# Optimization experiments

Hardware: AMD Instinct MI355X
Metric: run time of the kernel (lower is better)

## Reference

```python
import jax, jax.numpy as jnp
import numpy as np

N, E, F, H = 50000, 500000, 128, 128   # nodes, edges, in-features, hidden
L, R, B = 3, 8, 30                     # layers, relations, bases
G, C = 16, 8                           # graphs in batch, classes
EPS = 1e-5


def setup_inputs() -> dict:
    key = jax.random.key(0)
    ks = jax.random.split(key, 16)
    x = jax.random.normal(ks[0], (N, F), jnp.float32)
    edge_index = jax.random.randint(ks[1], (2, E), 0, N)
    edge_attr = jax.random.randint(ks[2], (E,), 0, R)
    batch = jnp.sort(jax.random.randint(ks[3], (N,), 0, G))
    # RGCN params (all layers share shapes since F == H)
    basis = jax.random.normal(ks[4], (L, B, H, H), jnp.float32) * 0.05
    comp = jax.random.normal(ks[5], (L, R, B), jnp.float32) * 0.2
    root = jax.random.normal(ks[6], (L, H, H), jnp.float32) * 0.05
    bias = jnp.zeros((L, H), jnp.float32)
    # BatchNorm (eval mode: running stats)
    bn1_gamma = jnp.ones((F,), jnp.float32)
    bn1_beta = jnp.zeros((F,), jnp.float32)
    bn1_mean = jax.random.normal(ks[7], (F,), jnp.float32) * 0.1
    bn1_var = jax.random.uniform(ks[8], (F,), jnp.float32, 0.5, 1.5)
    bn2_gamma = jnp.ones((H,), jnp.float32)
    bn2_beta = jnp.zeros((H,), jnp.float32)
    bn2_mean = jax.random.normal(ks[9], (H,), jnp.float32) * 0.1
    bn2_var = jax.random.uniform(ks[10], (H,), jnp.float32, 0.5, 1.5)
    fc1_w = jax.random.normal(ks[11], (H, H), jnp.float32) * 0.05
    fc1_b = jnp.zeros((H,), jnp.float32)
    fc2_w = jax.random.normal(ks[12], (H, C), jnp.float32) * 0.05
    fc2_b = jnp.zeros((C,), jnp.float32)
    return dict(x=x, edge_index=edge_index, edge_attr=edge_attr, batch=batch,
                bn1_gamma=bn1_gamma, bn1_beta=bn1_beta, bn1_mean=bn1_mean, bn1_var=bn1_var,
                basis=basis, comp=comp, root=root, bias=bias,
                bn2_gamma=bn2_gamma, bn2_beta=bn2_beta, bn2_mean=bn2_mean, bn2_var=bn2_var,
                fc1_w=fc1_w, fc1_b=fc1_b, fc2_w=fc2_w, fc2_b=fc2_b)


def _bn(x, gamma, beta, mean, var):
    return (x - mean) * jax.lax.rsqrt(var + EPS) * gamma + beta


def _rgcn_layer(x, basis_l, comp_l, root_l, bias_l, src, dst, edge_attr):
    # root transform + bias
    out = x @ root_l + bias_l
    # relation-wise basis-decomposed message passing, mean-aggregated per relation
    for r in range(R):
        W_r = jnp.einsum('b,bio->io', comp_l[r], basis_l)  # [H, H]
        xw = x @ W_r                                       # [N, H]
        mask = (edge_attr == r).astype(x.dtype)            # [E]
        msg = xw[src] * mask[:, None]                      # gather + mask
        agg = jax.ops.segment_sum(msg, dst, num_segments=N)
        deg = jax.ops.segment_sum(mask, dst, num_segments=N)
        out = out + agg / jnp.maximum(deg, 1.0)[:, None]
    return out


def reference(x, edge_index, edge_attr, batch,
              bn1_gamma, bn1_beta, bn1_mean, bn1_var,
              basis, comp, root, bias,
              bn2_gamma, bn2_beta, bn2_mean, bn2_var,
              fc1_w, fc1_b, fc2_w, fc2_b):
    src, dst = edge_index[0], edge_index[1]
    h = _bn(x, bn1_gamma, bn1_beta, bn1_mean, bn1_var)
    for l in range(L):
        h = jax.nn.relu(_rgcn_layer(h, basis[l], comp[l], root[l], bias[l], src, dst, edge_attr))
        # dropout is identity in eval mode
    # global mean pool per graph
    sums = jax.ops.segment_sum(h, batch, num_segments=G)            # [G, H]
    counts = jax.ops.segment_sum(jnp.ones((N,), h.dtype), batch, num_segments=G)
    g = sums / jnp.maximum(counts, 1.0)[:, None]
    g = _bn(g, bn2_gamma, bn2_beta, bn2_mean, bn2_var)
    # temporal_type == 'mean'
    v = jax.nn.relu(g.mean(axis=0))                                 # [H]
    v = jax.nn.relu(v @ fc1_w + fc1_b)
    logits = v @ fc2_w + fc2_b                                      # [C]
    return jax.nn.log_softmax(logits, axis=-1)
```

## Files before the change

kernel.cpp:

```cpp
#include <hip/hip_runtime.h>
#include <hip/hip_bf16.h>

#define NN 50000
#define NE 500000
#define HID 128
#define LAYERS 3
#define RELS 8
#define BASES 30
#define GRAPHS 16
#define CLASSES 8
#define EPSV 1e-5f
#define NOUT (HID * (RELS + 1))
#define SCAN_CHUNK 1024
#define SCAN_NBLK ((NN + SCAN_CHUNK - 1) / SCAN_CHUNK)
#define PCHUNK 128
#define NSTRIPE ((NN + 127) / 128)
#define NSG ((NSTRIPE + 7) / 8)

typedef __attribute__((ext_vector_type(8))) short short8;
typedef __attribute__((ext_vector_type(4))) float f32x4;
typedef __attribute__((ext_vector_type(2))) float f32x2;

__device__ __forceinline__ float bf2f(unsigned short u) {
    union { unsigned int i; float f; } x; x.i = ((unsigned int)u) << 16; return x.f;
}
__device__ __forceinline__ unsigned short f2bf(float f) {
    __hip_bfloat16 b = __float2bfloat16(f);
    return *(unsigned short*)&b;
}
template <bool HI>
__device__ __forceinline__ f32x2 fp8x2_2f(int u) {
    return __builtin_amdgcn_cvt_pk_f32_fp8(u, HI);
}
__device__ __forceinline__ int permf(int f) {
    return (f & 64) | ((f & 15) << 2) | ((f >> 4) & 3);
}
__device__ __forceinline__ int ipermf(int q) {
    return (q & 64) | ((q & 3) << 4) | ((q >> 2) & 15);
}
__device__ __forceinline__ void gload16(const void* g, void* l) {
    __builtin_amdgcn_global_load_lds(
        (const __attribute__((address_space(1))) unsigned int*)g,
        (__attribute__((address_space(3))) unsigned int*)l, 16, 0, 0);
}

__global__ __launch_bounds__(256) void build_wcat(const float* __restrict__ basis,
                                                  const float* __restrict__ comp,
                                                  const float* __restrict__ root,
                                                  unsigned short* __restrict__ wT) {
    int bid = blockIdx.x;
    int l = bid >> 6;
    int k0 = (bid & 63) << 1;
    __shared__ float cl[RELS * BASES];
    int tid = threadIdx.x;
    if (tid < RELS * BASES) cl[tid] = comp[l * RELS * BASES + tid];
    __syncthreads();
    int j = tid & 127;
    int k = k0 + (tid >> 7);
    int pk = permf(k);
    const float* bp = basis + ((size_t)l * BASES * HID + k) * HID + j;
    float acc[RELS];
#pragma unroll
    for (int r = 0; r < RELS; ++r) acc[r] = 0.f;
    for (int b = 0; b < BASES; ++b) {
        float v = bp[(size_t)b * HID * HID];
#pragma unroll
        for (int r = 0; r < RELS; ++r) acc[r] += cl[r * BASES + b] * v;
    }
    unsigned short* wl = wT + (size_t)l * NOUT * HID;
#pragma unroll
    for (int r = 0; r < RELS; ++r)
        wl[(size_t)((1 + r) * HID + j) * HID + pk] = f2bf(acc[r]);
    wl[(size_t)j * HID + pk] = f2bf(root[((size_t)l * HID + k) * HID + j]);
}

__global__ void bn1_kernel(const float* __restrict__ x, const float* __restrict__ gamma,
                           const float* __restrict__ beta, const float* __restrict__ mean,
                           const float* __restrict__ var, unsigned short* __restrict__ habf) {
    int idx = blockIdx.x * blockDim.x + threadIdx.x;
    if (idx >= NN * HID) return;
    int q = idx & (HID - 1);
    int n = idx >> 7;
    int f = ipermf(q);
    habf[idx] = f2bf((x[(n << 7) + f] - mean[f]) * rsqrtf(var[f] + EPSV) * gamma[f] + beta[f]);
}

__global__ void deg_kernel(const int* __restrict__ ei, const int* __restrict__ ea,
                           float* __restrict__ deg) {
    int e = blockIdx.x * blockDim.x + threadIdx.x;
    if (e >= NE) return;
    int dst = ei[NE + e];
    atomicAdd(&deg[(size_t)dst * RELS + ea[e]], 1.0f);
}

__global__ __launch_bounds__(256) void scan_partial(float* __restrict__ deg,
                                                    int* __restrict__ rowptr,
                                                    int* __restrict__ bsum) {
    __shared__ int ssc[256];
    int t = threadIdx.x;
    int base = blockIdx.x * SCAN_CHUNK + t * 4;
    int v[4];
#pragma unroll
    for (int j = 0; j < 4; ++j) {
        int node = base + j;
        if (node < NN) {
            float s = 0.f;
#pragma unroll
            for (int r = 0; r < RELS; ++r) {
                float d = deg[(size_t)node * RELS + r];
                s += d;
                deg[(size_t)node * RELS + r] = 1.0f / fmaxf(d, 1.0f);
            }
            v[j] = (int)(s + 0.5f);
        } else v[j] = 0;
    }
    int tsum = v[0] + v[1] + v[2] + v[3];
    ssc[t] = tsum;
    __syncthreads();
    for (int ofs = 1; ofs < 256; ofs <<= 1) {
        int add = (t >= ofs) ? ssc[t - ofs] : 0;
        __syncthreads();
        ssc[t] += add;
        __syncthreads();
    }
    int excl = ssc[t] - tsum;
    int e = 0;
#pragma unroll
    for (int j = 0; j < 4; ++j) {
        if (base + j < NN) rowptr[base + j] = excl + e;
        e += v[j];
    }
    if (t == 255) bsum[blockIdx.x] = ssc[255];
}

__global__ void scan_bsum(int* __restrict__ bsum) {
    if (threadIdx.x == 0) {
        int acc = 0;
        for (int b = 0; b < SCAN_NBLK; ++b) { int v = bsum[b]; bsum[b] = acc; acc += v; }
    }
}

__global__ __launch_bounds__(256) void scan_add(int* __restrict__ rowptr,
                                                const int* __restrict__ bsum) {
    int i = blockIdx.x * blockDim.x + threadIdx.x;
    if (i < NN) rowptr[i] += bsum[i >> 10];
    if (i == 0) rowptr[NN] = NE;
}

__global__ void fill_kernel(const int* __restrict__ ei, const int* __restrict__ ea,
                            const int* __restrict__ rowptr,
                            int* __restrict__ fillcnt, int* __restrict__ epk) {
    int e = blockIdx.x * blockDim.x + threadIdx.x;
    if (e >= NE) return;
    int src = ei[e];
    int dst = ei[NE + e];
    int r = ea[e];
    int pos = atomicAdd(&fillcnt[dst], 1);
    epk[rowptr[dst] + pos] = src | (r << 20);
}

__global__ __launch_bounds__(256) void gemm_mfma(const unsigned short* __restrict__ habf,
                                                 const unsigned short* __restrict__ wT,
                                                 const float* __restrict__ bias,
                                                 unsigned short* __restrict__ hnb,
                                                 unsigned char* __restrict__ xwb) {
    __shared__ __align__(16) unsigned short As[128 * 64];
    __shared__ __align__(16) unsigned short Bs[128 * 64];
    int bid = blockIdx.x;
    int sm8 = bid & 7;
    int rest = bid >> 3;
    int n0 = rest % (RELS + 1);
    int g = rest / (RELS + 1);
    int stripe = g * 8 + sm8;
    if (stripe >= NSTRIPE) return;
    int row0 = stripe * 128;

    int tid = threadIdx.x;
    int wave = tid >> 6, lane = tid & 63;
    int wm = (wave & 1) * 64, wn = (wave >> 1) * 64;
    int quad = lane >> 4, l16 = lane & 15;

    f32x4 acc[4][4];
#pragma unroll
    for (int i = 0; i < 4; ++i)
#pragma unroll
        for (int j = 0; j < 4; ++j) acc[i][j] = (f32x4){0.f, 0.f, 0.f, 0.f};

    int lr = lane >> 3;
    int lc = lane & 7;
    int sx = l16 & 7;

#pragma unroll
    for (int kh = 0; kh < 2; ++kh) {
#pragma unroll
        for (int q = 0; q < 4; ++q) {
            int rb = wave * 32 + q * 8;
            int r = rb + lr;
            int sc = (lc ^ (r & 7)) << 3;
            int ga = row0 + r; if (ga > NN - 1) ga = NN - 1;
            gload16(habf + (size_t)ga * HID + kh * 64 + sc, &As[rb * 64]);
            gload16(wT + (size_t)(n0 * 128 + r) * HID + kh * 64 + sc, &Bs[rb * 64]);
        }
        __syncthreads();
#pragma unroll
        for (int kc = 0; kc < 2; ++kc) {
            int ca = ((kc * 4 + quad) ^ sx) << 3;
            short8 a[4], b[4];
#pragma unroll
            for (int i = 0; i < 4; ++i) {
                a[i] = *(const short8*)&As[(wm + i * 16 + l16) * 64 + ca];
                b[i] = *(const short8*)&Bs[(wn + i * 16 + l16) * 64 + ca];
            }
#pragma unroll
            for (int i = 0; i < 4; ++i)
#pragma unroll
                for (int j = 0; j < 4; ++j)
                    acc[i][j] = __builtin_amdgcn_mfma_f32_16x16x32_bf16(a[i], b[j], acc[i][j], 0, 0, 0);
        }
        __syncthreads();
    }

    int pbase = wn + l16 * 4;
    if (n0 == 0) {
#pragma unroll
        for (int i = 0; i < 4; ++i)
#pragma unroll
            for (int reg = 0; reg < 4; ++reg) {
                int grow = row0 + wm + i * 16 + quad * 4 + reg;
                if (grow >= NN) continue;
                unsigned lo = (unsigned)f2bf(acc[i][0][reg] + bias[wn + l16]) |
                              ((unsigned)f2bf(acc[i][1][reg] + bias[wn + 16 + l16]) << 16);
                unsigned hi = (unsigned)f2bf(acc[i][2][reg] + bias[wn + 32 + l16]) |
                              ((unsigned)f2bf(acc[i][3][reg] + bias[wn + 48 + l16]) << 16);
                uint2 pk = {lo, hi};
                *(uint2*)(hnb + (size_t)grow * HID + pbase) = pk;
            }
    } else {
        int cbase = (n0 - 1) * 128;
#pragma unroll
        for (int i = 0; i < 4; ++i)
#pragma unroll
            for (int reg = 0; reg < 4; ++reg) {
                int grow = row0 + wm + i * 16 + quad * 4 + reg;
                if (grow >= NN) continue;
                unsigned w = (unsigned)__builtin_amdgcn_cvt_pk_fp8_f32(acc[i][0][reg], acc[i][1][reg], 0, false);
                w = (unsigned)__builtin_amdgcn_cvt_pk_fp8_f32(acc[i][2][reg], acc[i][3][reg], (int)w, true);
                *(unsigned*)(xwb + (size_t)grow * (RELS * HID) + cbase + pbase) = w;
            }
    }
}

__global__ __launch_bounds__(256) void aggregate_kernel(const int* __restrict__ rowptr,
                                                        const int* __restrict__ epk,
                                                        const float* __restrict__ invdeg,
                                                        const unsigned char* __restrict__ xwb,
                                                        const unsigned short* __restrict__ hnb,
                                                        unsigned short* __restrict__ habf) {
    int lane = threadIdx.x & 63;
    int half = lane >> 5;
    int hl = lane & 31;
    int node = (blockIdx.x << 3) + ((threadIdx.x >> 6) << 1) + half;
    if (node >= NN) return;
    int beg = rowptr[node], end = rowptr[node + 1];
    float dv = invdeg[(size_t)node * RELS + (hl & 7)];
    float a0 = 0.f, a1 = 0.f, a2 = 0.f, a3 = 0.f;
    int sbase = half << 5;
    for (int b0 = beg; b0 < end; b0 += 32) {
        int cnt = min(32, end - b0);
        int myp = 0;
        if (hl < cnt) myp = epk[b0 + hl];
        int j = 0;
        for (; j + 8 <= cnt; j += 8) {
            int p[8]; float s[8]; unsigned u[8];
#pragma unroll
            for (int t = 0; t < 8; ++t) p[t] = __shfl(myp, sbase + j + t);
#pragma unroll
            for (int t = 0; t < 8; ++t) s[t] = __shfl(dv, sbase + (p[t] >> 20));
#pragma unroll
            for (int t = 0; t < 8; ++t)
                u[t] = *(const unsigned*)(xwb + (size_t)(p[t] & 0xFFFFF) * (RELS * HID) + (p[t] >> 20) * HID + hl * 4);
#pragma unroll
            for (int t = 0; t < 8; ++t) {
                f32x2 lo = fp8x2_2f<false>((int)u[t]), hi = fp8x2_2f<true>((int)u[t]);
                a0 += lo.x * s[t]; a1 += lo.y * s[t]; a2 += hi.x * s[t]; a3 += hi.y * s[t];
            }
        }
        if (j + 4 <= cnt) {
            int p[4]; float s[4]; unsigned u[4];
#pragma unroll
            for (int t = 0; t < 4; ++t) p[t] = __shfl(myp, sbase + j + t);
#pragma unroll
            for (int t = 0; t < 4; ++t) s[t] = __shfl(dv, sbase + (p[t] >> 20));
#pragma unroll
            for (int t = 0; t < 4; ++t)
                u[t] = *(const unsigned*)(xwb + (size_t)(p[t] & 0xFFFFF) * (RELS * HID) + (p[t] >> 20) * HID + hl * 4);
#pragma unroll
            for (int t = 0; t < 4; ++t) {
                f32x2 lo = fp8x2_2f<false>((int)u[t]), hi = fp8x2_2f<true>((int)u[t]);
                a0 += lo.x * s[t]; a1 += lo.y * s[t]; a2 += hi.x * s[t]; a3 += hi.y * s[t];
            }
            j += 4;
        }
        for (; j < cnt; ++j) {
            int p = __shfl(myp, sbase + j);
            float s = __shfl(dv, sbase + (p >> 20));
            unsigned u = *(const unsigned*)(xwb + (size_t)(p & 0xFFFFF) * (RELS * HID) + (p >> 20) * HID + hl * 4);
            f32x2 lo = fp8x2_2f<false>((int)u), hi = fp8x2_2f<true>((int)u);
            a0 += lo.x * s; a1 += lo.y * s; a2 += hi.x * s; a3 += hi.y * s;
        }
    }
    const ushort2* hp = (const ushort2*)(hnb + (size_t)node * HID + hl * 4);
    ushort2 c0 = hp[0], c1 = hp[1];
    ushort2 o0, o1;
    o0.x = f2bf(fmaxf(bf2f(c0.x) + a0, 0.f));
    o0.y = f2bf(fmaxf(bf2f(c0.y) + a1, 0.f));
    o1.x = f2bf(fmaxf(bf2f(c1.x) + a2, 0.f));
    o1.y = f2bf(fmaxf(bf2f(c1.y) + a3, 0.f));
    ushort2* op = (ushort2*)(habf + (size_t)node * HID + hl * 4);
    op[0] = o0;
    op[1] = o1;
}

__global__ __launch_bounds__(256) void pool_kernel(const unsigned short* __restrict__ habf,
                                                   const int* __restrict__ batch,
                                                   float* __restrict__ psum,
                                                   float* __restrict__ pcnt) {
    int tid = threadIdx.x;
    int f = tid & 127;
    int sub = tid >> 7;
    int base = blockIdx.x * PCHUNK;
    float acc = 0.f, cnt = 0.f;
    int gcur = -1;
    for (int it = 0; it < PCHUNK / 2; ++it) {
        int node = base + it * 2 + sub;
        if (node >= NN) break;
        int g = batch[node];
        if (g != gcur) {
            if (gcur >= 0) {
                atomicAdd(&psum[gcur * HID + f], acc);
                if (f == 0) atomicAdd(&pcnt[gcur], cnt);
            }
            gcur = g; acc = 0.f; cnt = 0.f;
        }
        acc += bf2f(habf[(size_t)node * HID + f]);
        cnt += 1.f;
    }
    if (gcur >= 0) {
        atomicAdd(&psum[gcur * HID + f], acc);
        if (f == 0) atomicAdd(&pcnt[gcur], cnt);
    }
}

__global__ void head_kernel(const float* __restrict__ psum, const float* __restrict__ pcnt,
                            const float* __restrict__ g2, const float* __restrict__ b2,
                            const float* __restrict__ m2, const float* __restrict__ v2,
                            const float* __restrict__ fc1w, const float* __restrict__ fc1b,
                            const float* __restrict__ fc2w, const float* __restrict__ fc2b,
                            float* __restrict__ out) {
    __shared__ float v[HID];
    __shared__ float u[HID];
    __shared__ float lg[CLASSES];
    int j = threadIdx.x;
    int pj = permf(j);
    float acc = 0.f;
    for (int g = 0; g < GRAPHS; ++g) {
        float val = psum[g * HID + pj] / fmaxf(pcnt[g], 1.0f);
        val = (val - m2[j]) * rsqrtf(v2[j] + EPSV) * g2[j] + b2[j];
        acc += val;
    }
    v[j] = fmaxf(acc / (float)GRAPHS, 0.f);
    __syncthreads();
    float s = fc1b[j];
    for (int k = 0; k < HID; ++k) s += v[k] * fc1w[k * HID + j];
    u[j] = fmaxf(s, 0.f);
    __syncthreads();
    if (j < CLASSES) {
        float t = fc2b[j];
        for (int k = 0; k < HID; ++k) t += u[k] * fc2w[k * CLASSES + j];
        lg[j] = t;
    }
    __syncthreads();
    if (j < CLASSES) {
        float mx = lg[0];
        for (int c = 1; c < CLASSES; ++c) mx = fmaxf(mx, lg[c]);
        float se = 0.f;
        for (int c = 0; c < CLASSES; ++c) se += expf(lg[c] - mx);
        out[j] = lg[j] - mx - logf(se);
    }
}

extern "C" void kernel_launch(void* const* d_in, const int* in_sizes, int n_in,
                              void* d_out, int out_size, void* d_ws, size_t ws_size,
                              hipStream_t stream) {
    const float* x     = (const float*)d_in[0];
    const int*   ei    = (const int*)d_in[1];
    const int*   ea    = (const int*)d_in[2];
    const int*   batch = (const int*)d_in[3];
    const float* bn1g  = (const float*)d_in[4];
    const float* bn1b  = (const float*)d_in[5];
    const float* bn1m  = (const float*)d_in[6];
    const float* bn1v  = (const float*)d_in[7];
    const float* basis = (const float*)d_in[8];
    const float* comp  = (const float*)d_in[9];
    const float* root  = (const float*)d_in[10];
    const float* bias  = (const float*)d_in[11];
    const float* bn2g  = (const float*)d_in[12];
    const float* bn2b  = (const float*)d_in[13];
    const float* bn2m  = (const float*)d_in[14];
    const float* bn2v  = (const float*)d_in[15];
    const float* fc1w  = (const float*)d_in[16];
    const float* fc1b  = (const float*)d_in[17];
    const float* fc2w  = (const float*)d_in[18];
    const float* fc2b  = (const float*)d_in[19];

    float* ws = (float*)d_ws;
    size_t off = 0;
    unsigned short* wT = (unsigned short*)(ws + off); off += (size_t)LAYERS * NOUT * HID / 2;
    unsigned short* hnb  = (unsigned short*)(ws + off); off += (size_t)NN * HID / 2;
    unsigned short* habf = (unsigned short*)(ws + off); off += (size_t)NN * HID / 2;
    float* deg    = ws + off; off += (size_t)NN * RELS;
    float* psum   = ws + off; off += (size_t)GRAPHS * HID + GRAPHS;
    float* pcnt   = psum + GRAPHS * HID;
    int* rowptr   = (int*)(ws + off); off += (size_t)NN + 1;
    int* fillcnt  = (int*)(ws + off); off += (size_t)NN;
    int* bsum     = (int*)(ws + off); off += (size_t)SCAN_NBLK;
    int* epk      = (int*)(ws + off); off += (size_t)NE;
    off = (off + 3) & ~(size_t)3;
    unsigned char* xwb = (unsigned char*)(ws + off);
    off += (size_t)NN * RELS * HID / 4;
    if (ws_size < off * sizeof(float)) return;

    hipMemsetAsync(psum, 0, (GRAPHS * HID + GRAPHS) * sizeof(float), stream);
    hipMemsetAsync(deg, 0, (size_t)NN * RELS * sizeof(float), stream);
    hipMemsetAsync(fillcnt, 0, (size_t)NN * sizeof(int), stream);

    build_wcat<<<LAYERS * 64, 256, 0, stream>>>(basis, comp, root, wT);
    bn1_kernel<<<(NN * HID + 255) / 256, 256, 0, stream>>>(x, bn1g, bn1b, bn1m, bn1v, habf);

    deg_kernel<<<(NE + 255) / 256, 256, 0, stream>>>(ei, ea, deg);
    scan_partial<<<SCAN_NBLK, 256, 0, stream>>>(deg, rowptr, bsum);
    scan_bsum<<<1, 64, 0, stream>>>(bsum);
    scan_add<<<(NN + 255) / 256, 256, 0, stream>>>(rowptr, bsum);
    fill_kernel<<<(NE + 255) / 256, 256, 0, stream>>>(ei, ea, rowptr, fillcnt, epk);

    int gblocks = NSG * (RELS + 1) * 8;
    for (int l = 0; l < LAYERS; ++l) {
        gemm_mfma<<<gblocks, 256, 0, stream>>>(habf, wT + (size_t)l * NOUT * HID,
                                               bias + (size_t)l * HID, hnb, xwb);
        aggregate_kernel<<<(NN + 7) / 8, 256, 0, stream>>>(rowptr, epk, deg, xwb, hnb, habf);
    }

    pool_kernel<<<(NN + PCHUNK - 1) / PCHUNK, 256, 0, stream>>>(habf, batch, psum, pcnt);
    head_kernel<<<1, 128, 0, stream>>>(psum, pcnt, bn2g, bn2b, bn2m, bn2v,
                                       fc1w, fc1b, fc2w, fc2b, (float*)d_out);
}
```

Measured before the change: 397.1 us.

## Aggregate neighbor features per relation before transform in fused RGCN layer kernel

Replaces the transform-then-aggregate scheme (a GEMM writing 8 per-relation fp8 transformed features per node, then a gather kernel) with one fused kernel per layer. Each block of 64 destination nodes gathers and mean-aggregates raw bf16 neighbor features per relation using a (node,relation)-segmented CSR, then multiplies each aggregate by that relation's weight panel with MFMA, accumulating the root term, bias and ReLU in registers. This removes the large per-relation transformed-feature intermediate and its write and read traffic, and drops fp8 for bf16 inputs. In exchange each block runs nine serialized gather-then-MFMA phases with block barriers, has low occupancy given 48KB of LDS, and the CSR scan now covers eight times as many segments, so the bsum scan is widened to 512 threads.

New measurement: 488.8 us. 1.23x slower.

```diff
diff --git a/kernel.cpp b/kernel.cpp
--- a/kernel.cpp
+++ b/kernel.cpp
@@ -11,15 +11,15 @@
 #define CLASSES 8
 #define EPSV 1e-5f
 #define NOUT (HID * (RELS + 1))
+#define NSEG (NN * RELS)
 #define SCAN_CHUNK 1024
-#define SCAN_NBLK ((NN + SCAN_CHUNK - 1) / SCAN_CHUNK)
+#define SCAN_NBLK2 ((NSEG + SCAN_CHUNK - 1) / SCAN_CHUNK)
 #define PCHUNK 128
-#define NSTRIPE ((NN + 127) / 128)
-#define NSG ((NSTRIPE + 7) / 8)
+#define DTILE 64
+#define NDBLK ((NN + DTILE - 1) / DTILE)
 
 typedef __attribute__((ext_vector_type(8))) short short8;
 typedef __attribute__((ext_vector_type(4))) float f32x4;
-typedef __attribute__((ext_vector_type(2))) float f32x2;
 
 __device__ __forceinline__ float bf2f(unsigned short u) {
     union { unsigned int i; float f; } x; x.i = ((unsigned int)u) << 16; return x.f;
@@ -28,9 +28,11 @@
     __hip_bfloat16 b = __float2bfloat16(f);
     return *(unsigned short*)&b;
 }
-template <bool HI>
-__device__ __forceinline__ f32x2 fp8x2_2f(int u) {
-    return __builtin_amdgcn_cvt_pk_f32_fp8(u, HI);
+__device__ __forceinline__ float ubf_lo(unsigned w) {
+    union { unsigned i; float f; } t; t.i = w << 16; return t.f;
+}
+__device__ __forceinline__ float ubf_hi(unsigned w) {
+    union { unsigned i; float f; } t; t.i = w & 0xFFFF0000u; return t.f;
 }
 __device__ __forceinline__ int permf(int f) {
     return (f & 64) | ((f & 15) << 2) | ((f >> 4) & 3);
@@ -102,16 +104,11 @@
     int v[4];
 #pragma unroll
     for (int j = 0; j < 4; ++j) {
-        int node = base + j;
-        if (node < NN) {
-            float s = 0.f;
-#pragma unroll
-            for (int r = 0; r < RELS; ++r) {
-                float d = deg[(size_t)node * RELS + r];
-                s += d;
-                deg[(size_t)node * RELS + r] = 1.0f / fmaxf(d, 1.0f);
-            }
-            v[j] = (int)(s + 0.5f);
+        int seg = base + j;
+        if (seg < NSEG) {
+            float d = deg[seg];
+            v[j] = (int)(d + 0.5f);
+            deg[seg] = 1.0f / fmaxf(d, 1.0f);
         } else v[j] = 0;
     }
     int tsum = v[0] + v[1] + v[2] + v[3];
@@ -127,24 +124,32 @@
     int e = 0;
 #pragma unroll
     for (int j = 0; j < 4; ++j) {
-        if (base + j < NN) rowptr[base + j] = excl + e;
+        if (base + j < NSEG) rowptr[base + j] = excl + e;
         e += v[j];
     }
     if (t == 255) bsum[blockIdx.x] = ssc[255];
 }
 
-__global__ void scan_bsum(int* __restrict__ bsum) {
-    if (threadIdx.x == 0) {
-        int acc = 0;
-        for (int b = 0; b < SCAN_NBLK; ++b) { int v = bsum[b]; bsum[b] = acc; acc += v; }
-    }
+__global__ __launch_bounds__(512) void scan_bsum(int* __restrict__ bsum) {
+    __shared__ int s[512];
+    int t = threadIdx.x;
+    int v = (t < SCAN_NBLK2) ? bsum[t] : 0;
+    s[t] = v;
+    __syncthreads();
+    for (int o = 1; o < 512; o <<= 1) {
+        int a = (t >= o) ? s[t - o] : 0;
+        __syncthreads();
+        s[t] += a;
+        __syncthreads();
+    }
+    if (t < SCAN_NBLK2) bsum[t] = s[t] - v;
 }
 
 __global__ __launch_bounds__(256) void scan_add(int* __restrict__ rowptr,
                                                 const int* __restrict__ bsum) {
     int i = blockIdx.x * blockDim.x + threadIdx.x;
-    if (i < NN) rowptr[i] += bsum[i >> 10];
-    if (i == 0) rowptr[NN] = NE;
+    if (i < NSEG) rowptr[i] += bsum[i >> 10];
+    if (i == 0) rowptr[NSEG] = NE;
 }
 
 __global__ void fill_kernel(const int* __restrict__ ei, const int* __restrict__ ea,
@@ -153,172 +158,121 @@
     int e = blockIdx.x * blockDim.x + threadIdx.x;
     if (e >= NE) return;
     int src = ei[e];
-    int dst = ei[NE + e];
-    int r = ea[e];
-    int pos = atomicAdd(&fillcnt[dst], 1);
-    epk[rowptr[dst] + pos] = src | (r << 20);
-}
-
-__global__ __launch_bounds__(256) void gemm_mfma(const unsigned short* __restrict__ habf,
-                                                 const unsigned short* __restrict__ wT,
-                                                 const float* __restrict__ bias,
-                                                 unsigned short* __restrict__ hnb,
-                                                 unsigned char* __restrict__ xwb) {
-    __shared__ __align__(16) unsigned short As[128 * 64];
-    __shared__ __align__(16) unsigned short Bs[128 * 64];
-    int bid = blockIdx.x;
-    int sm8 = bid & 7;
-    int rest = bid >> 3;
-    int n0 = rest % (RELS + 1);
-    int g = rest / (RELS + 1);
-    int stripe = g * 8 + sm8;
-    if (stripe >= NSTRIPE) return;
-    int row0 = stripe * 128;
-
+    int seg = ei[NE + e] * RELS + ea[e];
+    int pos = atomicAdd(&fillcnt[seg], 1);
+    epk[rowptr[seg] + pos] = src;
+}
+
+__global__ __launch_bounds__(256) void rgcn_layer(const unsigned short* __restrict__ hin,
+                                                  const unsigned short* __restrict__ wTl,
+                                                  const float* __restrict__ bias,
+                                                  const int* __restrict__ rp2,
+                                                  const int* __restrict__ epk2,
+                                                  const float* __restrict__ invdeg,
+                                                  unsigned short* __restrict__ hout) {
+    __shared__ __align__(16) unsigned short As[DTILE * HID];
+    __shared__ __align__(16) unsigned short Bs[128 * HID];
+    int row0 = blockIdx.x * DTILE;
     int tid = threadIdx.x;
     int wave = tid >> 6, lane = tid & 63;
-    int wm = (wave & 1) * 64, wn = (wave >> 1) * 64;
     int quad = lane >> 4, l16 = lane & 15;
-
-    f32x4 acc[4][4];
+    int wn = wave * 32;
+    int ld = tid >> 2, tq = tid & 3;
+    int dst = row0 + ld;
+
+    f32x4 acc[4][2];
 #pragma unroll
     for (int i = 0; i < 4; ++i)
 #pragma unroll
-        for (int j = 0; j < 4; ++j) acc[i][j] = (f32x4){0.f, 0.f, 0.f, 0.f};
-
-    int lr = lane >> 3;
-    int lc = lane & 7;
-    int sx = l16 & 7;
-
-#pragma unroll
-    for (int kh = 0; kh < 2; ++kh) {
-#pragma unroll
-        for (int q = 0; q < 4; ++q) {
-            int rb = wave * 32 + q * 8;
-            int r = rb + lr;
-            int sc = (lc ^ (r & 7)) << 3;
-            int ga = row0 + r; if (ga > NN - 1) ga = NN - 1;
-            gload16(habf + (size_t)ga * HID + kh * 64 + sc, &As[rb * 64]);
-            gload16(wT + (size_t)(n0 * 128 + r) * HID + kh * 64 + sc, &Bs[rb * 64]);
-        }
-        __syncthreads();
-#pragma unroll
-        for (int kc = 0; kc < 2; ++kc) {
-            int ca = ((kc * 4 + quad) ^ sx) << 3;
-            short8 a[4], b[4];
-#pragma unroll
-            for (int i = 0; i < 4; ++i) {
-                a[i] = *(const short8*)&As[(wm + i * 16 + l16) * 64 + ca];
-                b[i] = *(const short8*)&Bs[(wn + i * 16 + l16) * 64 + ca];
+        for (int j = 0; j < 2; ++j) acc[i][j] = (f32x4){0.f, 0.f, 0.f, 0.f};
+
+    auto mfma_panel = [&]() {
+#pragma unroll
+        for (int kc = 0; kc < 4; ++kc) {
+            int ca = ((kc * 4 + quad) ^ (l16 & 7)) << 3;
+            short8 a[4], b[2];
+#pragma unroll
+            for (int i = 0; i < 4; ++i) a[i] = *(const short8*)&As[(i * 16 + l16) * HID + ca];
+#pragma unroll
+            for (int j = 0; j < 2; ++j) b[j] = *(const short8*)&Bs[(wn + j * 16 + l16) * HID + ca];
+#pragma unroll
+            for (int i = 0; i < 4; ++i)
+#pragma unroll
+                for (int j = 0; j < 2; ++j)
+                    acc[i][j] = __builtin_amdgcn_mfma_f32_16x16x32_bf16(a[i], b[j], acc[i][j], 0, 0, 0);
+        }
+    };
+
+#pragma unroll
+    for (int q = 0; q < 4; ++q) {
+        int rb = (wave << 4) + (q << 2);
+        int r = rb + (lane >> 4), c = lane & 15;
+        int ga = row0 + r; if (ga > NN - 1) ga = NN - 1;
+        gload16(hin + (size_t)ga * HID + ((c ^ (r & 7)) << 3), &As[rb * HID]);
+    }
+#pragma unroll
+    for (int q = 0; q < 8; ++q) {
+        int rb = (wave << 5) + (q << 2);
+        int r = rb + (lane >> 4), c = lane & 15;
+        gload16(wTl + (size_t)r * HID + ((c ^ (r & 7)) << 3), &Bs[rb * HID]);
+    }
+    __syncthreads();
+    mfma_panel();
+
+    for (int p = 1; p <= RELS; ++p) {
+        float ga[32];
+#pragma unroll
+        for (int i2 = 0; i2 < 32; ++i2) ga[i2] = 0.f;
+        float s = 0.f;
+        if (dst < NN) {
+            int seg = dst * RELS + (p - 1);
+            int beg = rp2[seg], end = rp2[seg + 1];
+            s = invdeg[seg];
+            for (int e = beg; e < end; ++e) {
+                int src = epk2[e];
+                const uint4* rp = (const uint4*)(hin + (size_t)src * HID + (tq << 5));
+                uint4 q0 = rp[0], q1 = rp[1], q2 = rp[2], q3 = rp[3];
+#pragma unroll
+                for (int q4 = 0; q4 < 4; ++q4) {
+                    uint4 u = (q4 == 0) ? q0 : (q4 == 1) ? q1 : (q4 == 2) ? q2 : q3;
+                    ga[q4 * 8 + 0] += ubf_lo(u.x); ga[q4 * 8 + 1] += ubf_hi(u.x);
+                    ga[q4 * 8 + 2] += ubf_lo(u.y); ga[q4 * 8 + 3] += ubf_hi(u.y);
+                    ga[q4 * 8 + 4] += ubf_lo(u.z); ga[q4 * 8 + 5] += ubf_hi(u.z);
+                    ga[q4 * 8 + 6] += ubf_lo(u.w); ga[q4 * 8 + 7] += ubf_hi(u.w);
+                }
             }
-#pragma unroll
-            for (int i = 0; i < 4; ++i)
-#pragma unroll
-                for (int j = 0; j < 4; ++j)
-                    acc[i][j] = __builtin_amdgcn_mfma_f32_16x16x32_bf16(a[i], b[j], acc[i][j], 0, 0, 0);
-        }
-        __syncthreads();
-    }
-
-    int pbase = wn + l16 * 4;
-    if (n0 == 0) {
-#pragma unroll
-        for (int i = 0; i < 4; ++i)
-#pragma unroll
-            for (int reg = 0; reg < 4; ++reg) {
-                int grow = row0 + wm + i * 16 + quad * 4 + reg;
-                if (grow >= NN) continue;
-                unsigned lo = (unsigned)f2bf(acc[i][0][reg] + bias[wn + l16]) |
-                              ((unsigned)f2bf(acc[i][1][reg] + bias[wn + 16 + l16]) << 16);
-                unsigned hi = (unsigned)f2bf(acc[i][2][reg] + bias[wn + 32 + l16]) |
-                              ((unsigned)f2bf(acc[i][3][reg] + bias[wn + 48 + l16]) << 16);
-                uint2 pk = {lo, hi};
-                *(uint2*)(hnb + (size_t)grow * HID + pbase) = pk;
-            }
-    } else {
-        int cbase = (n0 - 1) * 128;
-#pragma unroll
-        for (int i = 0; i < 4; ++i)
-#pragma unroll
-            for (int reg = 0; reg < 4; ++reg) {
-                int grow = row0 + wm + i * 16 + quad * 4 + reg;
-                if (grow >= NN) continue;
-                unsigned w = (unsigned)__builtin_amdgcn_cvt_pk_fp8_f32(acc[i][0][reg], acc[i][1][reg], 0, false);
-                w = (unsigned)__builtin_amdgcn_cvt_pk_fp8_f32(acc[i][2][reg], acc[i][3][reg], (int)w, true);
-                *(unsigned*)(xwb + (size_t)grow * (RELS * HID) + cbase + pbase) = w;
-            }
-    }
-}
-
-__global__ __launch_bounds__(256) void aggregate_kernel(const int* __restrict__ rowptr,
-                                                        const int* __restrict__ epk,
-                                                        const float* __restrict__ invdeg,
-                                                        const unsigned char* __restrict__ xwb,
-                                                        const unsigned short* __restrict__ hnb,
-                                                        unsigned short* __restrict__ habf) {
-    int lane = threadIdx.x & 63;
-    int half = lane >> 5;
-    int hl = lane & 31;
-    int node = (blockIdx.x << 3) + ((threadIdx.x >> 6) << 1) + half;
-    if (node >= NN) return;
-    int beg = rowptr[node], end = rowptr[node + 1];
-    float dv = invdeg[(size_t)node * RELS + (hl & 7)];
-    float a0 = 0.f, a1 = 0.f, a2 = 0.f, a3 = 0.f;
-    int sbase = half << 5;
-    for (int b0 = beg; b0 < end; b0 += 32) {
-        int cnt = min(32, end - b0);
-        int myp = 0;
-        if (hl < cnt) myp = epk[b0 + hl];
-        int j = 0;
-        for (; j + 8 <= cnt; j += 8) {
-            int p[8]; float s[8]; unsigned u[8];
-#pragma unroll
-            for (int t = 0; t < 8; ++t) p[t] = __shfl(myp, sbase + j + t);
-#pragma unroll
-            for (int t = 0; t < 8; ++t) s[t] = __shfl(dv, sbase + (p[t] >> 20));
-#pragma unroll
-            for (int t = 0; t < 8; ++t)
-                u[t] = *(const unsigned*)(xwb + (size_t)(p[t] & 0xFFFFF) * (RELS * HID) + (p[t] >> 20) * HID + hl * 4);
-#pragma unroll
-            for (int t = 0; t < 8; ++t) {
-                f32x2 lo = fp8x2_2f<false>((int)u[t]), hi = fp8x2_2f<true>((int)u[t]);
-                a0 += lo.x * s[t]; a1 += lo.y * s[t]; a2 += hi.x * s[t]; a3 += hi.y * s[t];
-            }
-        }
-        if (j + 4 <= cnt) {
-            int p[4]; float s[4]; unsigned u[4];
-#pragma unroll
-            for (int t = 0; t < 4; ++t) p[t] = __shfl(myp, sbase + j + t);
-#pragma unroll
-            for (int t = 0; t < 4; ++t) s[t] = __shfl(dv, sbase + (p[t] >> 20));
-#pragma unroll
-            for (int t = 0; t < 4; ++t)
-                u[t] = *(const unsigned*)(xwb + (size_t)(p[t] & 0xFFFFF) * (RELS * HID) + (p[t] >> 20) * HID + hl * 4);
-#pragma unroll
-            for (int t = 0; t < 4; ++t) {
-                f32x2 lo = fp8x2_2f<false>((int)u[t]), hi = fp8x2_2f<true>((int)u[t]);
-                a0 += lo.x * s[t]; a1 += lo.y * s[t]; a2 += hi.x * s[t]; a3 += hi.y * s[t];
-            }
-            j += 4;
-        }
-        for (; j < cnt; ++j) {
-            int p = __shfl(myp, sbase + j);
-            float s = __shfl(dv, sbase + (p >> 20));
-            unsigned u = *(const unsigned*)(xwb + (size_t)(p & 0xFFFFF) * (RELS * HID) + (p >> 20) * HID + hl * 4);
-            f32x2 lo = fp8x2_2f<false>((int)u), hi = fp8x2_2f<true>((int)u);
-            a0 += lo.x * s; a1 += lo.y * s; a2 += hi.x * s; a3 += hi.y * s;
-        }
-    }
-    const ushort2* hp = (const ushort2*)(hnb + (size_t)node * HID + hl * 4);
-    ushort2 c0 = hp[0], c1 = hp[1];
-    ushort2 o0, o1;
-    o0.x = f2bf(fmaxf(bf2f(c0.x) + a0, 0.f));
-    o0.y = f2bf(fmaxf(bf2f(c0.y) + a1, 0.f));
-    o1.x = f2bf(fmaxf(bf2f(c1.x) + a2, 0.f));
-    o1.y = f2bf(fmaxf(bf2f(c1.y) + a3, 0.f));
-    ushort2* op = (ushort2*)(habf + (size_t)node * HID + hl * 4);
-    op[0] = o0;
-    op[1] = o1;
+        }
+        __syncthreads();
+#pragma unroll
+        for (int cc = 0; cc < 4; ++cc) {
+            short8 v;
+#pragma unroll
+            for (int i2 = 0; i2 < 8; ++i2) v[i2] = (short)f2bf(ga[cc * 8 + i2] * s);
+            int c = (tq << 2) + cc;
+            *(short8*)&As[ld * HID + ((c ^ (ld & 7)) << 3)] = v;
+        }
+#pragma unroll
+        for (int q = 0; q < 8; ++q) {
+            int rb = (wave << 5) + (q << 2);
+            int r = rb + (lane >> 4), c = lane & 15;
+            gload16(wTl + (size_t)(p * 128 + r) * HID + ((c ^ (r & 7)) << 3), &Bs[rb * HID]);
+        }
+        __syncthreads();
+        mfma_panel();
+    }
+
+    int pb = ((wave & 2) << 5) + (l16 << 2) + ((wave & 1) << 1);
+    float b0 = bias[wn + l16], b1 = bias[wn + 16 + l16];
+#pragma unroll
+    for (int i = 0; i < 4; ++i)
+#pragma unroll
+        for (int reg = 0; reg < 4; ++reg) {
+            int grow = row0 + i * 16 + quad * 4 + reg;
+            if (grow >= NN) continue;
+            unsigned u = (unsigned)f2bf(fmaxf(acc[i][0][reg] + b0, 0.f))
+                       | ((unsigned)f2bf(fmaxf(acc[i][1][reg] + b1, 0.f)) << 16);
+            *(unsigned*)(hout + (size_t)grow * HID + pb) = u;
+        }
 }
 
 __global__ __launch_bounds__(256) void pool_kernel(const unsigned short* __restrict__ habf,
@@ -415,42 +369,40 @@
 
     float* ws = (float*)d_ws;
     size_t off = 0;
-    unsigned short* wT = (unsigned short*)(ws + off); off += (size_t)LAYERS * NOUT * HID / 2;
-    unsigned short* hnb  = (unsigned short*)(ws + off); off += (size_t)NN * HID / 2;
-    unsigned short* habf = (unsigned short*)(ws + off); off += (size_t)NN * HID / 2;
-    float* deg    = ws + off; off += (size_t)NN * RELS;
+    unsigned short* wT  = (unsigned short*)(ws + off); off += (size_t)LAYERS * NOUT * HID / 2;
+    unsigned short* hb0 = (unsigned short*)(ws + off); off += (size_t)NN * HID / 2;
+    unsigned short* hb1 = (unsigned short*)(ws + off); off += (size_t)NN * HID / 2;
+    float* deg    = ws + off; off += (size_t)NSEG;
     float* psum   = ws + off; off += (size_t)GRAPHS * HID + GRAPHS;
     float* pcnt   = psum + GRAPHS * HID;
-    int* rowptr   = (int*)(ws + off); off += (size_t)NN + 1;
-    int* fillcnt  = (int*)(ws + off); off += (size_t)NN;
-    int* bsum     = (int*)(ws + off); off += (size_t)SCAN_NBLK;
-    int* epk      = (int*)(ws + off); off += (size_t)NE;
-    off = (off + 3) & ~(size_t)3;
-    unsigned char* xwb = (unsigned char*)(ws + off);
-    off += (size_t)NN * RELS * HID / 4;
+    int* rowptr2  = (int*)(ws + off); off += (size_t)NSEG + 1;
+    int* fillcnt2 = (int*)(ws + off); off += (size_t)NSEG;
+    int* bsum     = (int*)(ws + off); off += (size_t)SCAN_NBLK2;
+    int* epk2     = (int*)(ws + off); off += (size_t)NE;
     if (ws_size < off * sizeof(float)) return;
 
     hipMemsetAsync(psum, 0, (GRAPHS * HID + GRAPHS) * sizeof(float), stream);
-    hipMemsetAsync(deg, 0, (size_t)NN * RELS * sizeof(float), stream);
-    hipMemsetAsync(fillcnt, 0, (size_t)NN * sizeof(int), stream);
+    hipMemsetAsync(deg, 0, (size_t)NSEG * sizeof(float), stream);
+    hipMemsetAsync(fillcnt2, 0, (size_t)NSEG * sizeof(int), stream);
 
     build_wcat<<<LAYERS * 64, 256, 0, stream>>>(basis, comp, root, wT);
-    bn1_kernel<<<(NN * HID + 255) / 256, 256, 0, stream>>>(x, bn1g, bn1b, bn1m, bn1v, habf);
+    bn1_kernel<<<(NN * HID + 255) / 256, 256, 0, stream>>>(x, bn1g, bn1b, bn1m, bn1v, hb0);
 
     deg_kernel<<<(NE + 255) / 256, 256, 0, stream>>>(ei, ea, deg);
-    scan_partial<<<SCAN_NBLK, 256, 0, stream>>>(deg, rowptr, bsum);
-    scan_bsum<<<1, 64, 0, stream>>>(bsum);
-    scan_add<<<(NN + 255) / 256, 256, 0, stream>>>(rowptr, bsum);
-    fill_kernel<<<(NE + 255) / 256, 256, 0, stream>>>(ei, ea, rowptr, fillcnt, epk);
-
-    int gblocks = NSG * (RELS + 1) * 8;
+    scan_partial<<<SCAN_NBLK2, 256, 0, stream>>>(deg, rowptr2, bsum);
+    scan_bsum<<<1, 512, 0, stream>>>(bsum);
+    scan_add<<<(NSEG + 255) / 256, 256, 0, stream>>>(rowptr2, bsum);
+    fill_kernel<<<(NE + 255) / 256, 256, 0, stream>>>(ei, ea, rowptr2, fillcnt2, epk2);
+
+    const unsigned short* hin = hb0;
+    unsigned short* hout = hb1;
     for (int l = 0; l < LAYERS; ++l) {
-        gemm_mfma<<<gblocks, 256, 0, stream>>>(habf, wT + (size_t)l * NOUT * HID,
-                                               bias + (size_t)l * HID, hnb, xwb);
-        aggregate_kernel<<<(NN + 7) / 8, 256, 0, stream>>>(rowptr, epk, deg, xwb, hnb, habf);
-    }
-
-    pool_kernel<<<(NN + PCHUNK - 1) / PCHUNK, 256, 0, stream>>>(habf, batch, psum, pcnt);
+        rgcn_layer<<<NDBLK, 256, 0, stream>>>(hin, wT + (size_t)l * NOUT * HID,
+                                              bias + (size_t)l * HID, rowptr2, epk2, deg, hout);
+        const unsigned short* t = hin; hin = hout; hout = (unsigned short*)t;
+    }
+
+    pool_kernel<<<(NN + PCHUNK - 1) / PCHUNK, 256, 0, stream>>>(hin, batch, psum, pcnt);
     head_kernel<<<1, 128, 0, stream>>>(psum, pcnt, bn2g, bn2b, bn2m, bn2v,
                                        fc1w, fc1b, fc2w, fc2b, (float*)d_out);
 }
```

## Reuse A tile in LDS across three output column blocks, read B directly from global

Applied to the files above, without the earlier changes.

The GEMM block now loads the full 128x128 activation tile into LDS once and loops over three of the nine output column blocks, instead of reloading A for every column block. The weight operand is read straight from global memory (cached) into registers rather than staged through LDS, which also removes the per-k-half syncthreads. The grid shrinks to a third as many blocks. This cuts redundant activation loads, at the cost of uncoalesced-ish direct B loads, higher register pressure, and less parallelism per launch.

Result: slower. 440.5 us (+10.9%).

```diff
diff --git a/kernel.cpp b/kernel.cpp
--- a/kernel.cpp
+++ b/kernel.cpp
@@ -164,14 +164,13 @@
                                                  const float* __restrict__ bias,
                                                  unsigned short* __restrict__ hnb,
                                                  unsigned char* __restrict__ xwb) {
-    __shared__ __align__(16) unsigned short As[128 * 64];
-    __shared__ __align__(16) unsigned short Bs[128 * 64];
+    __shared__ __align__(16) unsigned short As[128 * HID];
     int bid = blockIdx.x;
-    int sm8 = bid & 7;
-    int rest = bid >> 3;
-    int n0 = rest % (RELS + 1);
-    int g = rest / (RELS + 1);
-    int stripe = g * 8 + sm8;
+    int sg = bid / 24;
+    int rem = bid - sg * 24;
+    int g = rem >> 3;
+    int s8 = rem & 7;
+    int stripe = sg * 8 + s8;
     if (stripe >= NSTRIPE) return;
     int row0 = stripe * 128;
 
@@ -179,74 +178,76 @@
     int wave = tid >> 6, lane = tid & 63;
     int wm = (wave & 1) * 64, wn = (wave >> 1) * 64;
     int quad = lane >> 4, l16 = lane & 15;
-
-    f32x4 acc[4][4];
-#pragma unroll
-    for (int i = 0; i < 4; ++i)
-#pragma unroll
-        for (int j = 0; j < 4; ++j) acc[i][j] = (f32x4){0.f, 0.f, 0.f, 0.f};
-
-    int lr = lane >> 3;
-    int lc = lane & 7;
     int sx = l16 & 7;
 
-#pragma unroll
-    for (int kh = 0; kh < 2; ++kh) {
-#pragma unroll
-        for (int q = 0; q < 4; ++q) {
-            int rb = wave * 32 + q * 8;
-            int r = rb + lr;
-            int sc = (lc ^ (r & 7)) << 3;
-            int ga = row0 + r; if (ga > NN - 1) ga = NN - 1;
-            gload16(habf + (size_t)ga * HID + kh * 64 + sc, &As[rb * 64]);
-            gload16(wT + (size_t)(n0 * 128 + r) * HID + kh * 64 + sc, &Bs[rb * 64]);
-        }
-        __syncthreads();
-#pragma unroll
-        for (int kc = 0; kc < 2; ++kc) {
+    int sr = lane >> 4;
+    int sp = lane & 15;
+#pragma unroll
+    for (int q = 0; q < 8; ++q) {
+        int rb = wave * 32 + q * 4;
+        int r = rb + sr;
+        int sc = (sp ^ (r & 7)) << 3;
+        int ga = row0 + r; if (ga > NN - 1) ga = NN - 1;
+        gload16(habf + (size_t)ga * HID + sc, &As[rb * HID]);
+    }
+    __syncthreads();
+
+#pragma unroll
+    for (int nn = 0; nn < 3; ++nn) {
+        int n0 = g * 3 + nn;
+        f32x4 acc[4][4];
+#pragma unroll
+        for (int i = 0; i < 4; ++i)
+#pragma unroll
+            for (int j = 0; j < 4; ++j) acc[i][j] = (f32x4){0.f, 0.f, 0.f, 0.f};
+
+#pragma unroll
+        for (int kc = 0; kc < 4; ++kc) {
+            uint4 b4[4];
+#pragma unroll
+            for (int j = 0; j < 4; ++j)
+                b4[j] = *(const uint4*)(wT + (size_t)(n0 * 128 + wn + j * 16 + l16) * HID
+                                        + ((kc * 4 + quad) << 3));
             int ca = ((kc * 4 + quad) ^ sx) << 3;
-            short8 a[4], b[4];
-#pragma unroll
-            for (int i = 0; i < 4; ++i) {
-                a[i] = *(const short8*)&As[(wm + i * 16 + l16) * 64 + ca];
-                b[i] = *(const short8*)&Bs[(wn + i * 16 + l16) * 64 + ca];
-            }
+            short8 a[4];
 #pragma unroll
             for (int i = 0; i < 4; ++i)
+                a[i] = *(const short8*)&As[(wm + i * 16 + l16) * HID + ca];
+#pragma unroll
+            for (int i = 0; i < 4; ++i)
 #pragma unroll
                 for (int j = 0; j < 4; ++j)
-                    acc[i][j] = __builtin_amdgcn_mfma_f32_16x16x32_bf16(a[i], b[j], acc[i][j], 0, 0, 0);
-        }
-        __syncthreads();
-    }
-
-    int pbase = wn + l16 * 4;
-    if (n0 == 0) {
-#pragma unroll
-        for (int i = 0; i < 4; ++i)
-#pragma unroll
-            for (int reg = 0; reg < 4; ++reg) {
-                int grow = row0 + wm + i * 16 + quad * 4 + reg;
-                if (grow >= NN) continue;
-                unsigned lo = (unsigned)f2bf(acc[i][0][reg] + bias[wn + l16]) |
-                              ((unsigned)f2bf(acc[i][1][reg] + bias[wn + 16 + l16]) << 16);
-                unsigned hi = (unsigned)f2bf(acc[i][2][reg] + bias[wn + 32 + l16]) |
-                              ((unsigned)f2bf(acc[i][3][reg] + bias[wn + 48 + l16]) << 16);
-                uint2 pk = {lo, hi};
-                *(uint2*)(hnb + (size_t)grow * HID + pbase) = pk;
-            }
-    } else {
-        int cbase = (n0 - 1) * 128;
-#pragma unroll
-        for (int i = 0; i < 4; ++i)
-#pragma unroll
-            for (int reg = 0; reg < 4; ++reg) {
-                int grow = row0 + wm + i * 16 + quad * 4 + reg;
-                if (grow >= NN) continue;
-                unsigned w = (unsigned)__builtin_amdgcn_cvt_pk_fp8_f32(acc[i][0][reg], acc[i][1][reg], 0, false);
-                w = (unsigned)__builtin_amdgcn_cvt_pk_fp8_f32(acc[i][2][reg], acc[i][3][reg], (int)w, true);
-                *(unsigned*)(xwb + (size_t)grow * (RELS * HID) + cbase + pbase) = w;
-            }
+                    acc[i][j] = __builtin_amdgcn_mfma_f32_16x16x32_bf16(a[i], *(const short8*)&b4[j], acc[i][j], 0, 0, 0);
+        }
+
+        int pbase = wn + l16 * 4;
+        if (n0 == 0) {
+#pragma unroll
+            for (int i = 0; i < 4; ++i)
+#pragma unroll
+                for (int reg = 0; reg < 4; ++reg) {
+                    int grow = row0 + wm + i * 16 + quad * 4 + reg;
+                    if (grow >= NN) continue;
+                    unsigned lo = (unsigned)f2bf(acc[i][0][reg] + bias[wn + l16]) |
+                                  ((unsigned)f2bf(acc[i][1][reg] + bias[wn + 16 + l16]) << 16);
+                    unsigned hi = (unsigned)f2bf(acc[i][2][reg] + bias[wn + 32 + l16]) |
+                                  ((unsigned)f2bf(acc[i][3][reg] + bias[wn + 48 + l16]) << 16);
+                    uint2 pk = {lo, hi};
+                    *(uint2*)(hnb + (size_t)grow * HID + pbase) = pk;
+                }
+        } else {
+            int cbase = (n0 - 1) * 128;
+#pragma unroll
+            for (int i = 0; i < 4; ++i)
+#pragma unroll
+                for (int reg = 0; reg < 4; ++reg) {
+                    int grow = row0 + wm + i * 16 + quad * 4 + reg;
+                    if (grow >= NN) continue;
+                    unsigned w = (unsigned)__builtin_amdgcn_cvt_pk_fp8_f32(acc[i][0][reg], acc[i][1][reg], 0, false);
+                    w = (unsigned)__builtin_amdgcn_cvt_pk_fp8_f32(acc[i][2][reg], acc[i][3][reg], (int)w, true);
+                    *(unsigned*)(xwb + (size_t)grow * (RELS * HID) + cbase + pbase) = w;
+                }
+        }
     }
 }
 
@@ -443,7 +444,7 @@
     scan_add<<<(NN + 255) / 256, 256, 0, stream>>>(rowptr, bsum);
     fill_kernel<<<(NE + 255) / 256, 256, 0, stream>>>(ei, ea, rowptr, fillcnt, epk);
 
-    int gblocks = NSG * (RELS + 1) * 8;
+    int gblocks = NSG * 24;
     for (int l = 0; l < LAYERS; ++l) {
         gemm_mfma<<<gblocks, 256, 0, stream>>>(habf, wT + (size_t)l * NOUT * HID,
                                                bias + (size_t)l * HID, hnb, xwb);
```
